# Optimization experiments

Measured on AMD Instinct MI355X. Metric: run time of the kernel, lower is better.

## Reference

```python
import jax, jax.numpy as jnp
import numpy as np

N_COMBIN, N_DEV, CONT, VOCAB, EMB = 50000, 100000, 62, 1000, 16
B, K, H, OUT, NCLS = 8192, 64, 4, 16, 1
FEAT = CONT + 2 * EMB  # 94
ALPHA = 0.2  # leaky relu slope


def setup_inputs() -> dict:
    key = jax.random.key(0)
    ks = jax.random.split(key, 32)
    rn = lambda k, shape, s=0.05: (jax.random.normal(k, shape, dtype=jnp.float32) * s)
    inp = {
        "combin_cont": jax.random.normal(ks[0], (N_COMBIN, CONT), jnp.float32),
        "combin_cat": jax.random.randint(ks[1], (N_COMBIN, 2), 0, VOCAB),
        "device_cont": jax.random.normal(ks[2], (N_DEV, CONT), jnp.float32),
        "device_cat": jax.random.randint(ks[3], (N_DEV, 2), 0, VOCAB),
        "combin_idx": jax.random.randint(ks[4], (B,), 0, N_COMBIN),
        "device_idx": jax.random.randint(ks[5], (B,), 0, N_DEV),
        "neighbor_idx": jax.random.randint(ks[6], (B, K), 0, N_DEV),
        "ce0": rn(ks[7], (VOCAB, EMB), 1.0),
        "ce1": rn(ks[8], (VOCAB, EMB), 1.0),
        "de0": rn(ks[9], (VOCAB, EMB), 1.0),
        "de1": rn(ks[10], (VOCAB, EMB), 1.0),
        "Wc": rn(ks[11], (H, FEAT, OUT)),
        "bc": rn(ks[12], (H, OUT)),
        "Wd": rn(ks[13], (H, FEAT, OUT)),
        "bd": rn(ks[14], (H, OUT)),
        "aW": rn(ks[15], (H, 2 * OUT)),
        "ab": rn(ks[16], (H,)),
        "W1": rn(ks[17], (H * OUT, OUT)),
        "b1": rn(ks[18], (OUT,)),
        "W2": rn(ks[19], (OUT + 2 * FEAT, 64)),
        "b2": rn(ks[20], (64,)),
        "W3": rn(ks[21], (64, 32)),
        "b3": rn(ks[22], (32,)),
        "W4": rn(ks[23], (32, NCLS)),
        "b4": rn(ks[24], (NCLS,)),
    }
    return inp


def reference(combin_cont, combin_cat, device_cont, device_cat,
              combin_idx, device_idx, neighbor_idx,
              ce0, ce1, de0, de1,
              Wc, bc, Wd, bd, aW, ab,
              W1, b1, W2, b2, W3, b3, W4, b4):
    # concat_embed_feats for device nodes: [N_dev, FEAT]
    dev_feats = jnp.concatenate(
        [device_cont, de0[device_cat[:, 0]], de1[device_cat[:, 1]]], axis=1)
    # combin batch features: [B, FEAT]
    cc = combin_cat[combin_idx]
    comb_batch = jnp.concatenate(
        [combin_cont[combin_idx], ce0[cc[:, 0]], ce1[cc[:, 1]]], axis=1)
    dev_batch = dev_feats[device_idx]            # [B, FEAT]
    neibr = dev_feats[neighbor_idx]              # [B, K, FEAT]

    # multi-head GAT attention (all heads vectorized)
    h_c = jnp.einsum('bf,hfo->bho', comb_batch, Wc) + bc[None]          # [B,H,OUT]
    h_n = jnp.einsum('bkf,hfo->bhko', neibr, Wd) + bd[None, :, None]    # [B,H,K,OUT]
    a1, a2 = aW[:, :OUT], aW[:, OUT:]
    e = (jnp.einsum('bho,ho->bh', h_c, a1)[:, :, None]
         + jnp.einsum('bhko,ho->bhk', h_n, a2)
         + ab[None, :, None])                                           # [B,H,K]
    e = jax.nn.leaky_relu(e, negative_slope=ALPHA)
    attn = jax.nn.softmax(e, axis=-1)
    head_out = jax.nn.elu(jnp.einsum('bhk,bhko->bho', attn, h_n))       # [B,H,OUT]
    attn_feats = head_out.reshape(head_out.shape[0], H * OUT) @ W1 + b1  # [B,OUT]

    fusion = jnp.concatenate([comb_batch, dev_batch, attn_feats], axis=1)
    x = jax.nn.relu(fusion @ W2 + b2)   # dropout is identity in eval
    x = jax.nn.relu(x @ W3 + b3)
    return jax.nn.sigmoid(x @ W4 + b4)  # [B, NCLS]
```

## Files before the change

kernel.cpp:

```cpp
#include <hip/hip_runtime.h>
#include <cmath>

#define NDEV   100000
#define NBATCH 8192
#define CONTF  62
#define EMB    16
#define FEAT   94
#define KNBR   64
#define NH     4
#define OUTD   16
#define HOUT   64
#define FUS    204
#define ALPHA  0.2f

#define NDEVG  1563
#define NCOMBG 128


template <typename T>
__device__ __forceinline__ const T* uniform_ptr(const T* p) {
  uint64_t v = (uint64_t)(uintptr_t)p;
  uint32_t lo = __builtin_amdgcn_readfirstlane((uint32_t)v);
  uint32_t hi = __builtin_amdgcn_readfirstlane((uint32_t)(v >> 32));
  return (const T*)(uintptr_t)(((uint64_t)hi << 32) | lo);
}

__device__ __forceinline__ void fma16(float acc[OUTD], float x,
                                      const float* __restrict__ Wg, int f) {
  const float4* wr = reinterpret_cast<const float4*>(Wg + f * OUTD);
  const float4 w0 = wr[0], w1 = wr[1], w2 = wr[2], w3 = wr[3];
  acc[0]  = fmaf(x, w0.x, acc[0]);  acc[1]  = fmaf(x, w0.y, acc[1]);
  acc[2]  = fmaf(x, w0.z, acc[2]);  acc[3]  = fmaf(x, w0.w, acc[3]);
  acc[4]  = fmaf(x, w1.x, acc[4]);  acc[5]  = fmaf(x, w1.y, acc[5]);
  acc[6]  = fmaf(x, w1.z, acc[6]);  acc[7]  = fmaf(x, w1.w, acc[7]);
  acc[8]  = fmaf(x, w2.x, acc[8]);  acc[9]  = fmaf(x, w2.y, acc[9]);
  acc[10] = fmaf(x, w2.z, acc[10]); acc[11] = fmaf(x, w2.w, acc[11]);
  acc[12] = fmaf(x, w3.x, acc[12]); acc[13] = fmaf(x, w3.y, acc[13]);
  acc[14] = fmaf(x, w3.z, acc[14]); acc[15] = fmaf(x, w3.w, acc[15]);
}

__global__ __launch_bounds__(256, 4) void k_feat(
    const float* __restrict__ device_cont, const int* __restrict__ device_cat,
    const float* __restrict__ de0, const float* __restrict__ de1,
    const float* __restrict__ Wd, const float* __restrict__ bd,
    const float* __restrict__ combin_cont, const int* __restrict__ combin_cat,
    const int* __restrict__ combin_idx,
    const float* __restrict__ ce0, const float* __restrict__ ce1,
    const float* __restrict__ Wc, const float* __restrict__ bc,
    const float* __restrict__ aW,
    float* __restrict__ h_d, float* __restrict__ e_d, float* __restrict__ e_c) {
  const int lane = threadIdx.x & 63;
  const int g = __builtin_amdgcn_readfirstlane((int)(threadIdx.x >> 6));
  const int blk = blockIdx.x;
  const bool devp = blk < NDEVG;

  const int row = (devp ? blk : blk - NDEVG) * 64 + lane;
  const bool valid = devp ? (row < NDEV) : true;
  const int rr = valid ? row : NDEV - 1;

  const int src = devp ? rr : combin_idx[rr];
  const int2 cat = reinterpret_cast<const int2*>(devp ? device_cat : combin_cat)[src];
  const float* __restrict__ crow =
      (devp ? device_cont : combin_cont) + (size_t)src * CONTF;
  const float* __restrict__ e0p = (devp ? de0 : ce0) + (size_t)cat.x * EMB;
  const float* __restrict__ e1p = (devp ? de1 : ce1) + (size_t)cat.y * EMB;

  const float* Wg = uniform_ptr(devp ? Wd : Wc) + (size_t)g * FEAT * OUTD;
  const float* bg = uniform_ptr(devp ? bd : bc) + g * OUTD;
  const float* ag = uniform_ptr(aW) + g * 2 * OUTD + (devp ? OUTD : 0);

  float acc[OUTD];
#pragma unroll
  for (int o = 0; o < OUTD; ++o) acc[o] = bg[o];

#pragma unroll
  for (int c = 0; c < 7; ++c) {
    const float2* p = reinterpret_cast<const float2*>(crow + c * 8);
    const float2 a0 = p[0], a1 = p[1], a2 = p[2], a3 = p[3];
    const float xs[8] = {a0.x, a0.y, a1.x, a1.y, a2.x, a2.y, a3.x, a3.y};
#pragma unroll
    for (int k = 0; k < 8; ++k) fma16(acc, xs[k], Wg, c * 8 + k);
  }
  {
    const float2* p = reinterpret_cast<const float2*>(crow + 56);
    const float2 a0 = p[0], a1 = p[1], a2 = p[2];
    const float xs[6] = {a0.x, a0.y, a1.x, a1.y, a2.x, a2.y};
#pragma unroll
    for (int k = 0; k < 6; ++k) fma16(acc, xs[k], Wg, 56 + k);
  }
  {
    const float4* p = reinterpret_cast<const float4*>(e0p);
    const float4 a0 = p[0], a1 = p[1], a2 = p[2], a3 = p[3];
    const float xs[16] = {a0.x, a0.y, a0.z, a0.w, a1.x, a1.y, a1.z, a1.w,
                          a2.x, a2.y, a2.z, a2.w, a3.x, a3.y, a3.z, a3.w};
#pragma unroll
    for (int k = 0; k < 16; ++k) fma16(acc, xs[k], Wg, CONTF + k);
  }
  {
    const float4* p = reinterpret_cast<const float4*>(e1p);
    const float4 a0 = p[0], a1 = p[1], a2 = p[2], a3 = p[3];
    const float xs[16] = {a0.x, a0.y, a0.z, a0.w, a1.x, a1.y, a1.z, a1.w,
                          a2.x, a2.y, a2.z, a2.w, a3.x, a3.y, a3.z, a3.w};
#pragma unroll
    for (int k = 0; k < 16; ++k) fma16(acc, xs[k], Wg, CONTF + EMB + k);
  }

  float ev = 0.f;
#pragma unroll
  for (int o = 0; o < OUTD; ++o) ev = fmaf(acc[o], ag[o], ev);

  if (devp) {
    if (valid) {
      float4* hr = reinterpret_cast<float4*>(h_d + (size_t)row * HOUT + g * OUTD);
      hr[0] = make_float4(acc[0], acc[1], acc[2], acc[3]);
      hr[1] = make_float4(acc[4], acc[5], acc[6], acc[7]);
      hr[2] = make_float4(acc[8], acc[9], acc[10], acc[11]);
      hr[3] = make_float4(acc[12], acc[13], acc[14], acc[15]);
      e_d[(size_t)row * NH + g] = ev;
    }
  } else {
    e_c[(size_t)row * NH + g] = ev;
  }
}

__global__ __launch_bounds__(256, 4) void k_attn(
    const int* __restrict__ neighbor_idx, const int* __restrict__ device_idx,
    const int* __restrict__ device_cat, const float* __restrict__ device_cont,
    const float* __restrict__ de0, const float* __restrict__ de1,
    const int* __restrict__ combin_idx, const int* __restrict__ combin_cat,
    const float* __restrict__ combin_cont,
    const float* __restrict__ ce0, const float* __restrict__ ce1,
    const float* __restrict__ h_d, const float* __restrict__ e_d,
    const float* __restrict__ e_c, const float* __restrict__ ab,
    const float* __restrict__ W1, const float* __restrict__ b1,
    float* __restrict__ fus) {
  __shared__ __align__(16) float pb[4][NH][68];
  __shared__ __align__(16) int   nb[4][KNBR];
  __shared__ float hb[4][HOUT];
  __shared__ float afb[4][OUTD];

  const int lane = threadIdx.x & 63;
  const int wid  = __builtin_amdgcn_readfirstlane((int)(threadIdx.x >> 6));
  const int b    = blockIdx.x * 4 + wid;

  const int nk = neighbor_idx[(size_t)b * KNBR + lane];
  const float4 ed4 = *reinterpret_cast<const float4*>(e_d + (size_t)nk * NH);
  const float4 ec4 = *reinterpret_cast<const float4*>(e_c + (size_t)b * NH);
  const float4 ab4 = *reinterpret_cast<const float4*>(ab);

  float v0 = ec4.x + ed4.x + ab4.x;
  float v1 = ec4.y + ed4.y + ab4.y;
  float v2 = ec4.z + ed4.z + ab4.z;
  float v3 = ec4.w + ed4.w + ab4.w;
  v0 = v0 > 0.f ? v0 : ALPHA * v0;
  v1 = v1 > 0.f ? v1 : ALPHA * v1;
  v2 = v2 > 0.f ? v2 : ALPHA * v2;
  v3 = v3 > 0.f ? v3 : ALPHA * v3;

  float m0 = v0, m1 = v1, m2 = v2, m3 = v3;
#pragma unroll
  for (int msk = 1; msk < 64; msk <<= 1) {
    m0 = fmaxf(m0, __shfl_xor(m0, msk));
    m1 = fmaxf(m1, __shfl_xor(m1, msk));
    m2 = fmaxf(m2, __shfl_xor(m2, msk));
    m3 = fmaxf(m3, __shfl_xor(m3, msk));
  }
  float p0 = expf(v0 - m0), p1 = expf(v1 - m1), p2 = expf(v2 - m2), p3 = expf(v3 - m3);
  float s0 = p0, s1 = p1, s2 = p2, s3 = p3;
#pragma unroll
  for (int msk = 1; msk < 64; msk <<= 1) {
    s0 += __shfl_xor(s0, msk);
    s1 += __shfl_xor(s1, msk);
    s2 += __shfl_xor(s2, msk);
    s3 += __shfl_xor(s3, msk);
  }
  p0 /= s0; p1 /= s1; p2 /= s2; p3 /= s3;

  pb[wid][0][lane] = p0;
  pb[wid][1][lane] = p1;
  pb[wid][2][lane] = p2;
  pb[wid][3][lane] = p3;
  nb[wid][lane]    = nk;
  __syncthreads();

  {
    const int q = lane >> 4, c4 = lane & 15;
    const int hq = c4 >> 2;
    float ax = 0.f, ay = 0.f, az = 0.f, aw = 0.f;
#pragma unroll
    for (int t = 0; t < 16; ++t) {
      const int n   = nb[wid][q * 16 + t];
      const float p = pb[wid][hq][q * 16 + t];
      const float4 hv =
          *reinterpret_cast<const float4*>(h_d + (size_t)n * HOUT + 4 * c4);
      ax = fmaf(p, hv.x, ax);
      ay = fmaf(p, hv.y, ay);
      az = fmaf(p, hv.z, az);
      aw = fmaf(p, hv.w, aw);
    }
#pragma unroll
    for (int msk = 16; msk < 64; msk <<= 1) {
      ax += __shfl_xor(ax, msk);
      ay += __shfl_xor(ay, msk);
      az += __shfl_xor(az, msk);
      aw += __shfl_xor(aw, msk);
    }
    if (q == 0) {
      ax = ax > 0.f ? ax : expm1f(ax);
      ay = ay > 0.f ? ay : expm1f(ay);
      az = az > 0.f ? az : expm1f(az);
      aw = aw > 0.f ? aw : expm1f(aw);
      *reinterpret_cast<float4*>(&hb[wid][4 * c4]) = make_float4(ax, ay, az, aw);
    }
  }
  __syncthreads();

  {
    const int j = lane & 15, gg = lane >> 4;
    float part = 0.f;
#pragma unroll
    for (int t = 0; t < 16; ++t)
      part = fmaf(hb[wid][gg * 16 + t], W1[(gg * 16 + t) * OUTD + j], part);
    part += __shfl_xor(part, 16);
    part += __shfl_xor(part, 32);
    if (lane < 16) afb[wid][lane] = part + b1[lane];
  }
  __syncthreads();

  const int ci = combin_idx[b];
  const int cc0 = combin_cat[2 * ci], cc1 = combin_cat[2 * ci + 1];
  const int didx = device_idx[b];
  const int dc0 = device_cat[2 * didx], dc1 = device_cat[2 * didx + 1];
  float* __restrict__ frow = fus + (size_t)b * FUS;
#pragma unroll
  for (int t = 0; t < 4; ++t) {
    const int i = lane + t * 64;
    if (i < FUS) {
      float v;
      if (i < 62)       v = combin_cont[(size_t)ci * CONTF + i];
      else if (i < 78)  v = ce0[(size_t)cc0 * EMB + (i - 62)];
      else if (i < 94)  v = ce1[(size_t)cc1 * EMB + (i - 78)];
      else if (i < 156) v = device_cont[(size_t)didx * CONTF + (i - 94)];
      else if (i < 172) v = de0[(size_t)dc0 * EMB + (i - 156)];
      else if (i < 188) v = de1[(size_t)dc1 * EMB + (i - 172)];
      else              v = afb[wid][i - 188];
      frow[i] = v;
    }
  }
}

__global__ __launch_bounds__(256) void k_mlp(
    const float* __restrict__ fus,
    const float* __restrict__ W2, const float* __restrict__ b2,
    const float* __restrict__ W3, const float* __restrict__ b3,
    const float* __restrict__ W4, const float* __restrict__ b4,
    float* __restrict__ out) {
  __shared__ __align__(16) float x1w[4][4][64];
  const int lane = threadIdx.x & 63;
  const int wid  = __builtin_amdgcn_readfirstlane((int)(threadIdx.x >> 6));
  const int w    = blockIdx.x * 4 + wid;
  const int r0   = w * 4;

  const float* rp0 = uniform_ptr(fus + (size_t)(r0 + 0) * FUS);
  const float* rp1 = uniform_ptr(fus + (size_t)(r0 + 1) * FUS);
  const float* rp2 = uniform_ptr(fus + (size_t)(r0 + 2) * FUS);
  const float* rp3 = uniform_ptr(fus + (size_t)(r0 + 3) * FUS);

  float acc[4];
  const float bj = b2[lane];
#pragma unroll
  for (int r = 0; r < 4; ++r) acc[r] = bj;

#pragma unroll 1
  for (int c = 0; c < 25; ++c) {
    const int f0 = c * 8;
#pragma unroll
    for (int k = 0; k < 8; ++k) {
      const float wv = W2[(f0 + k) * 64 + lane];
      acc[0] = fmaf(rp0[f0 + k], wv, acc[0]);
      acc[1] = fmaf(rp1[f0 + k], wv, acc[1]);
      acc[2] = fmaf(rp2[f0 + k], wv, acc[2]);
      acc[3] = fmaf(rp3[f0 + k], wv, acc[3]);
    }
  }
#pragma unroll
  for (int k = 0; k < 4; ++k) {
    const float wv = W2[(200 + k) * 64 + lane];
    acc[0] = fmaf(rp0[200 + k], wv, acc[0]);
    acc[1] = fmaf(rp1[200 + k], wv, acc[1]);
    acc[2] = fmaf(rp2[200 + k], wv, acc[2]);
    acc[3] = fmaf(rp3[200 + k], wv, acc[3]);
  }
#pragma unroll
  for (int r = 0; r < 4; ++r) x1w[wid][r][lane] = fmaxf(acc[r], 0.f);

  const int m = lane & 31, rh = lane >> 5;
  float x2[2];
#pragma unroll
  for (int r = 0; r < 2; ++r) x2[r] = b3[m];
#pragma unroll 2
  for (int j4 = 0; j4 < 16; ++j4) {
    const float w30 = W3[(4 * j4 + 0) * 32 + m];
    const float w31 = W3[(4 * j4 + 1) * 32 + m];
    const float w32 = W3[(4 * j4 + 2) * 32 + m];
    const float w33 = W3[(4 * j4 + 3) * 32 + m];
#pragma unroll
    for (int r = 0; r < 2; ++r) {
      const float4 xv = *reinterpret_cast<const float4*>(&x1w[wid][rh * 2 + r][4 * j4]);
      x2[r] = fmaf(xv.x, w30, x2[r]);
      x2[r] = fmaf(xv.y, w31, x2[r]);
      x2[r] = fmaf(xv.z, w32, x2[r]);
      x2[r] = fmaf(xv.w, w33, x2[r]);
    }
  }
  const float w4 = W4[m];
  float part[2];
#pragma unroll
  for (int r = 0; r < 2; ++r) part[r] = fmaxf(x2[r], 0.f) * w4;
#pragma unroll
  for (int msk = 1; msk < 32; msk <<= 1) {
#pragma unroll
    for (int r = 0; r < 2; ++r) part[r] += __shfl_xor(part[r], msk);
  }
  if (m == 0) {
    const float bb = b4[0];
#pragma unroll
    for (int r = 0; r < 2; ++r) {
      const float z = part[r] + bb;
      out[(size_t)(r0 + rh * 2 + r)] = 1.f / (1.f + expf(-z));
    }
  }
}

extern "C" void kernel_launch(void* const* d_in, const int* in_sizes, int n_in,
                              void* d_out, int out_size, void* d_ws, size_t ws_size,
                              hipStream_t stream) {
  const float* combin_cont  = (const float*)d_in[0];
  const int*   combin_cat   = (const int*)d_in[1];
  const float* device_cont  = (const float*)d_in[2];
  const int*   device_cat   = (const int*)d_in[3];
  const int*   combin_idx   = (const int*)d_in[4];
  const int*   device_idx   = (const int*)d_in[5];
  const int*   neighbor_idx = (const int*)d_in[6];
  const float* ce0 = (const float*)d_in[7];
  const float* ce1 = (const float*)d_in[8];
  const float* de0 = (const float*)d_in[9];
  const float* de1 = (const float*)d_in[10];
  const float* Wc  = (const float*)d_in[11];
  const float* bc  = (const float*)d_in[12];
  const float* Wd  = (const float*)d_in[13];
  const float* bd  = (const float*)d_in[14];
  const float* aW  = (const float*)d_in[15];
  const float* ab  = (const float*)d_in[16];
  const float* W1  = (const float*)d_in[17];
  const float* b1  = (const float*)d_in[18];
  const float* W2  = (const float*)d_in[19];
  const float* b2  = (const float*)d_in[20];
  const float* W3  = (const float*)d_in[21];
  const float* b3  = (const float*)d_in[22];
  const float* W4  = (const float*)d_in[23];
  const float* b4  = (const float*)d_in[24];

  float* ws  = (float*)d_ws;
  float* h_d = ws;
  float* e_d = ws + 6400000;
  float* e_c = ws + 6800000;
  float* fus = ws + 6832768;

  k_feat<<<NDEVG + NCOMBG, 256, 0, stream>>>(
      device_cont, device_cat, de0, de1, Wd, bd,
      combin_cont, combin_cat, combin_idx, ce0, ce1, Wc, bc, aW,
      h_d, e_d, e_c);
  k_attn<<<2048, 256, 0, stream>>>(
      neighbor_idx, device_idx, device_cat, device_cont, de0, de1,
      combin_idx, combin_cat, combin_cont, ce0, ce1,
      h_d, e_d, e_c, ab, W1, b1, fus);
  k_mlp<<<512, 256, 0, stream>>>(fus, W2, b2, W3, b3, W4, b4, (float*)d_out);
}
```

Baseline: 191.1 us.

## Store device head projections in bf16 and split MLP layer-1 across wave pairs

The per-device projected features h_d are now written as bf16 instead of fp32, which halves the 25.6MB intermediate write in k_feat and the random neighbor gathers in k_attn. The gather now uses 16-byte loads of 8 bf16 values per lane. Separately, k_mlp splits the 204-wide first layer across two waves that reduce through shared memory, and launches twice as many blocks for more parallelism. The bf16 storage adds rounding error to the attention aggregation, and the MLP split adds block-level synchronization.

After: 186.1 us. -2.6%, faster.

```diff
diff --git a/kernel.cpp b/kernel.cpp
--- a/kernel.cpp
+++ b/kernel.cpp
@@ -16,6 +16,9 @@
 #define NDEVG  1563
 #define NCOMBG 128
 
+typedef unsigned short ushortT;
+typedef ushortT ushort8v __attribute__((ext_vector_type(8)));
+
 
 template <typename T>
 __device__ __forceinline__ const T* uniform_ptr(const T* p) {
@@ -23,6 +26,15 @@
   uint32_t lo = __builtin_amdgcn_readfirstlane((uint32_t)v);
   uint32_t hi = __builtin_amdgcn_readfirstlane((uint32_t)(v >> 32));
   return (const T*)(uintptr_t)(((uint64_t)hi << 32) | lo);
+}
+
+__device__ __forceinline__ float bf2f(ushortT u) {
+  return __uint_as_float(((unsigned int)u) << 16);
+}
+__device__ __forceinline__ ushortT f2bf(float f) {
+  unsigned int i = __float_as_uint(f);
+  unsigned int r = i + 0x7FFFu + ((i >> 16) & 1u);
+  return (ushortT)(r >> 16);
 }
 
 __device__ __forceinline__ void fma16(float acc[OUTD], float x,
@@ -48,7 +60,7 @@
     const float* __restrict__ ce0, const float* __restrict__ ce1,
     const float* __restrict__ Wc, const float* __restrict__ bc,
     const float* __restrict__ aW,
-    float* __restrict__ h_d, float* __restrict__ e_d, float* __restrict__ e_c) {
+    ushortT* __restrict__ h_bf, float* __restrict__ e_d, float* __restrict__ e_c) {
   const int lane = threadIdx.x & 63;
   const int g = __builtin_amdgcn_readfirstlane((int)(threadIdx.x >> 6));
   const int blk = blockIdx.x;
@@ -111,11 +123,12 @@
 
   if (devp) {
     if (valid) {
-      float4* hr = reinterpret_cast<float4*>(h_d + (size_t)row * HOUT + g * OUTD);
-      hr[0] = make_float4(acc[0], acc[1], acc[2], acc[3]);
-      hr[1] = make_float4(acc[4], acc[5], acc[6], acc[7]);
-      hr[2] = make_float4(acc[8], acc[9], acc[10], acc[11]);
-      hr[3] = make_float4(acc[12], acc[13], acc[14], acc[15]);
+      ushort8v v0, v1;
+#pragma unroll
+      for (int o = 0; o < 8; ++o) { v0[o] = f2bf(acc[o]); v1[o] = f2bf(acc[8 + o]); }
+      ushort8v* dst = reinterpret_cast<ushort8v*>(h_bf + (size_t)row * HOUT + g * OUTD);
+      dst[0] = v0;
+      dst[1] = v1;
       e_d[(size_t)row * NH + g] = ev;
     }
   } else {
@@ -130,7 +143,7 @@
     const int* __restrict__ combin_idx, const int* __restrict__ combin_cat,
     const float* __restrict__ combin_cont,
     const float* __restrict__ ce0, const float* __restrict__ ce1,
-    const float* __restrict__ h_d, const float* __restrict__ e_d,
+    const ushortT* __restrict__ h_bf, const float* __restrict__ e_d,
     const float* __restrict__ e_c, const float* __restrict__ ab,
     const float* __restrict__ W1, const float* __restrict__ b1,
     float* __restrict__ fus) {
@@ -184,33 +197,32 @@
   __syncthreads();
 
   {
-    const int q = lane >> 4, c4 = lane & 15;
-    const int hq = c4 >> 2;
-    float ax = 0.f, ay = 0.f, az = 0.f, aw = 0.f;
-#pragma unroll
-    for (int t = 0; t < 16; ++t) {
-      const int n   = nb[wid][q * 16 + t];
-      const float p = pb[wid][hq][q * 16 + t];
-      const float4 hv =
-          *reinterpret_cast<const float4*>(h_d + (size_t)n * HOUT + 4 * c4);
-      ax = fmaf(p, hv.x, ax);
-      ay = fmaf(p, hv.y, ay);
-      az = fmaf(p, hv.z, az);
-      aw = fmaf(p, hv.w, aw);
-    }
-#pragma unroll
-    for (int msk = 16; msk < 64; msk <<= 1) {
-      ax += __shfl_xor(ax, msk);
-      ay += __shfl_xor(ay, msk);
-      az += __shfl_xor(az, msk);
-      aw += __shfl_xor(aw, msk);
+    const int q = lane >> 3, c8 = lane & 7;
+    const int hq = c8 >> 1;
+    float a[8];
+#pragma unroll
+    for (int i = 0; i < 8; ++i) a[i] = 0.f;
+#pragma unroll
+    for (int t = 0; t < 8; ++t) {
+      const int k   = q * 8 + t;
+      const int n   = nb[wid][k];
+      const float p = pb[wid][hq][k];
+      const ushort8v hv =
+          *reinterpret_cast<const ushort8v*>(h_bf + (size_t)n * HOUT + c8 * 8);
+#pragma unroll
+      for (int i = 0; i < 8; ++i) a[i] = fmaf(p, bf2f(hv[i]), a[i]);
+    }
+#pragma unroll
+    for (int msk = 8; msk < 64; msk <<= 1) {
+#pragma unroll
+      for (int i = 0; i < 8; ++i) a[i] += __shfl_xor(a[i], msk);
     }
     if (q == 0) {
-      ax = ax > 0.f ? ax : expm1f(ax);
-      ay = ay > 0.f ? ay : expm1f(ay);
-      az = az > 0.f ? az : expm1f(az);
-      aw = aw > 0.f ? aw : expm1f(aw);
-      *reinterpret_cast<float4*>(&hb[wid][4 * c4]) = make_float4(ax, ay, az, aw);
+#pragma unroll
+      for (int i = 0; i < 8; ++i) a[i] = a[i] > 0.f ? a[i] : expm1f(a[i]);
+      float4* hp = reinterpret_cast<float4*>(&hb[wid][c8 * 8]);
+      hp[0] = make_float4(a[0], a[1], a[2], a[3]);
+      hp[1] = make_float4(a[4], a[5], a[6], a[7]);
     }
   }
   __syncthreads();
@@ -255,80 +267,65 @@
     const float* __restrict__ W3, const float* __restrict__ b3,
     const float* __restrict__ W4, const float* __restrict__ b4,
     float* __restrict__ out) {
-  __shared__ __align__(16) float x1w[4][4][64];
-  const int lane = threadIdx.x & 63;
-  const int wid  = __builtin_amdgcn_readfirstlane((int)(threadIdx.x >> 6));
-  const int w    = blockIdx.x * 4 + wid;
-  const int r0   = w * 4;
-
-  const float* rp0 = uniform_ptr(fus + (size_t)(r0 + 0) * FUS);
-  const float* rp1 = uniform_ptr(fus + (size_t)(r0 + 1) * FUS);
-  const float* rp2 = uniform_ptr(fus + (size_t)(r0 + 2) * FUS);
-  const float* rp3 = uniform_ptr(fus + (size_t)(r0 + 3) * FUS);
+  __shared__ __align__(16) float part[4][4][64];
+  __shared__ __align__(16) float x1s[2][4][64];
+  const int tid  = threadIdx.x;
+  const int lane = tid & 63;
+  const int wid  = __builtin_amdgcn_readfirstlane((int)(tid >> 6));
+  const int pair = wid >> 1, half = wid & 1;
+  const int r0   = blockIdx.x * 8 + pair * 4;
+  const int f0   = half * 102;
+
+  const float* rp0 = uniform_ptr(fus + (size_t)(r0 + 0) * FUS + f0);
+  const float* rp1 = uniform_ptr(fus + (size_t)(r0 + 1) * FUS + f0);
+  const float* rp2 = uniform_ptr(fus + (size_t)(r0 + 2) * FUS + f0);
+  const float* rp3 = uniform_ptr(fus + (size_t)(r0 + 3) * FUS + f0);
 
   float acc[4];
-  const float bj = b2[lane];
+  const float bj = half ? 0.f : b2[lane];
 #pragma unroll
   for (int r = 0; r < 4; ++r) acc[r] = bj;
 
 #pragma unroll 1
-  for (int c = 0; c < 25; ++c) {
-    const int f0 = c * 8;
-#pragma unroll
-    for (int k = 0; k < 8; ++k) {
-      const float wv = W2[(f0 + k) * 64 + lane];
-      acc[0] = fmaf(rp0[f0 + k], wv, acc[0]);
-      acc[1] = fmaf(rp1[f0 + k], wv, acc[1]);
-      acc[2] = fmaf(rp2[f0 + k], wv, acc[2]);
-      acc[3] = fmaf(rp3[f0 + k], wv, acc[3]);
-    }
-  }
-#pragma unroll
-  for (int k = 0; k < 4; ++k) {
-    const float wv = W2[(200 + k) * 64 + lane];
-    acc[0] = fmaf(rp0[200 + k], wv, acc[0]);
-    acc[1] = fmaf(rp1[200 + k], wv, acc[1]);
-    acc[2] = fmaf(rp2[200 + k], wv, acc[2]);
-    acc[3] = fmaf(rp3[200 + k], wv, acc[3]);
-  }
-#pragma unroll
-  for (int r = 0; r < 4; ++r) x1w[wid][r][lane] = fmaxf(acc[r], 0.f);
-
-  const int m = lane & 31, rh = lane >> 5;
-  float x2[2];
-#pragma unroll
-  for (int r = 0; r < 2; ++r) x2[r] = b3[m];
+  for (int c = 0; c < 17; ++c) {
+#pragma unroll
+    for (int k = 0; k < 6; ++k) {
+      const int f = c * 6 + k;
+      const float wv = W2[(f0 + f) * 64 + lane];
+      acc[0] = fmaf(rp0[f], wv, acc[0]);
+      acc[1] = fmaf(rp1[f], wv, acc[1]);
+      acc[2] = fmaf(rp2[f], wv, acc[2]);
+      acc[3] = fmaf(rp3[f], wv, acc[3]);
+    }
+  }
+#pragma unroll
+  for (int r = 0; r < 4; ++r) part[wid][r][lane] = acc[r];
+  __syncthreads();
+
+  if (half == 0) {
+#pragma unroll
+    for (int r = 0; r < 4; ++r)
+      x1s[pair][r][lane] = fmaxf(part[wid][r][lane] + part[wid + 1][r][lane], 0.f);
+  }
+  __syncthreads();
+
+  const int row = tid >> 5, m = tid & 31;
+  const int pr = row >> 2, rr = row & 3;
+  float x2 = b3[m];
 #pragma unroll 2
   for (int j4 = 0; j4 < 16; ++j4) {
-    const float w30 = W3[(4 * j4 + 0) * 32 + m];
-    const float w31 = W3[(4 * j4 + 1) * 32 + m];
-    const float w32 = W3[(4 * j4 + 2) * 32 + m];
-    const float w33 = W3[(4 * j4 + 3) * 32 + m];
-#pragma unroll
-    for (int r = 0; r < 2; ++r) {
-      const float4 xv = *reinterpret_cast<const float4*>(&x1w[wid][rh * 2 + r][4 * j4]);
-      x2[r] = fmaf(xv.x, w30, x2[r]);
-      x2[r] = fmaf(xv.y, w31, x2[r]);
-      x2[r] = fmaf(xv.z, w32, x2[r]);
-      x2[r] = fmaf(xv.w, w33, x2[r]);
-    }
-  }
-  const float w4 = W4[m];
-  float part[2];
-#pragma unroll
-  for (int r = 0; r < 2; ++r) part[r] = fmaxf(x2[r], 0.f) * w4;
-#pragma unroll
-  for (int msk = 1; msk < 32; msk <<= 1) {
-#pragma unroll
-    for (int r = 0; r < 2; ++r) part[r] += __shfl_xor(part[r], msk);
-  }
+    const float4 xv = *reinterpret_cast<const float4*>(&x1s[pr][rr][4 * j4]);
+    x2 = fmaf(xv.x, W3[(4 * j4 + 0) * 32 + m], x2);
+    x2 = fmaf(xv.y, W3[(4 * j4 + 1) * 32 + m], x2);
+    x2 = fmaf(xv.z, W3[(4 * j4 + 2) * 32 + m], x2);
+    x2 = fmaf(xv.w, W3[(4 * j4 + 3) * 32 + m], x2);
+  }
+  float p3r = fmaxf(x2, 0.f) * W4[m];
+#pragma unroll
+  for (int msk = 1; msk < 32; msk <<= 1) p3r += __shfl_xor(p3r, msk);
   if (m == 0) {
-    const float bb = b4[0];
-#pragma unroll
-    for (int r = 0; r < 2; ++r) {
-      const float z = part[r] + bb;
-      out[(size_t)(r0 + rh * 2 + r)] = 1.f / (1.f + expf(-z));
-    }
+    const float z = p3r + b4[0];
+    out[(size_t)(blockIdx.x * 8 + row)] = 1.f / (1.f + expf(-z));
   }
 }
 
@@ -362,18 +359,18 @@
   const float* b4  = (const float*)d_in[24];
 
   float* ws  = (float*)d_ws;
-  float* h_d = ws;
-  float* e_d = ws + 6400000;
-  float* e_c = ws + 6800000;
-  float* fus = ws + 6832768;
+  ushortT* h_bf = (ushortT*)ws;
+  float* e_d = ws + 3200000;
+  float* e_c = ws + 3600000;
+  float* fus = ws + 3632768;
 
   k_feat<<<NDEVG + NCOMBG, 256, 0, stream>>>(
       device_cont, device_cat, de0, de1, Wd, bd,
       combin_cont, combin_cat, combin_idx, ce0, ce1, Wc, bc, aW,
-      h_d, e_d, e_c);
+      h_bf, e_d, e_c);
   k_attn<<<2048, 256, 0, stream>>>(
       neighbor_idx, device_idx, device_cat, device_cont, de0, de1,
       combin_idx, combin_cat, combin_cont, ce0, ce1,
-      h_d, e_d, e_c, ab, W1, b1, fus);
-  k_mlp<<<512, 256, 0, stream>>>(fus, W2, b2, W3, b3, W4, b4, (float*)d_out);
-}
+      h_bf, e_d, e_c, ab, W1, b1, fus);
+  k_mlp<<<1024, 256, 0, stream>>>(fus, W2, b2, W3, b3, W4, b4, (float*)d_out);
+}
```
